# Kernel tuning notes

Hardware: AMD Instinct MI355X
Metric: run time of the kernel (lower is better)

The kernel has to match this reference:

```python
import jax, jax.numpy as jnp
import numpy as np

N = 100000
E = 1600000
IN_C, HID_C, OUT_C = 128, 128, 64


def setup_inputs() -> dict:
    key = jax.random.key(0)
    ks = jax.random.split(key, 8)
    x = jax.random.normal(ks[0], (N, IN_C), dtype=jnp.float32)
    edge_index = jax.random.randint(ks[1], (2, E), 0, N, dtype=jnp.int64)

    def glorot(k, fan_in, fan_out):
        s = jnp.sqrt(6.0 / (fan_in + fan_out))
        return jax.random.uniform(k, (fan_in, fan_out), jnp.float32, -s, s)

    W1 = glorot(ks[2], IN_C, HID_C)
    b1 = jnp.zeros((HID_C,), jnp.float32)
    W2 = glorot(ks[3], HID_C, HID_C)
    b2 = jnp.zeros((HID_C,), jnp.float32)
    W3 = glorot(ks[4], HID_C, OUT_C)
    b3 = jnp.zeros((OUT_C,), jnp.float32)
    return {"x": x, "edge_index": edge_index,
            "W1": W1, "b1": b1, "W2": W2, "b2": b2, "W3": W3, "b3": b3}


def _gcn_norm(row, col, n_nodes):
    # symmetric normalization, add_self_loops=False (PyG gcn_norm)
    deg = jax.ops.segment_sum(jnp.ones(row.shape[0], jnp.float32), col, num_segments=n_nodes)
    dinv = jnp.where(deg > 0, jax.lax.rsqrt(jnp.maximum(deg, 1.0)), 0.0)
    dinv = jnp.where(deg > 0, deg ** -0.5, 0.0)
    return dinv[row] * dinv[col]  # [E]


def _gcn_conv(x, row, col, norm, W, b):
    h = x @ W                                # [N, F_out] dense GEMM first (PyG order)
    msg = h[row] * norm[:, None]             # gather + scale, [E, F_out]
    out = jax.ops.segment_sum(msg, col, num_segments=x.shape[0])  # scatter-add
    return out + b


def reference(x, edge_index, W1, b1, W2, b2, W3, b3):
    row, col = edge_index[0], edge_index[1]
    norm = _gcn_norm(row, col, x.shape[0])
    h = jax.nn.relu(_gcn_conv(x, row, col, norm, W1, b1))   # dropout is identity in eval
    h = jax.nn.relu(_gcn_conv(h, row, col, norm, W2, b2))
    out = _gcn_conv(h, row, col, norm, W3, b3)
    return out
```

## Files before the change

### kernel.cpp

```cpp
#include <hip/hip_runtime.h>
#include <hip/hip_bf16.h>
#include <hip/hip_fp16.h>


#define K_DIM 128
#define SCAN_CHUNK 1024

typedef _Float16 f16x8 __attribute__((ext_vector_type(8)));
typedef float f32x4 __attribute__((ext_vector_type(4)));
typedef const __attribute__((address_space(1))) void gbl_void;
typedef __attribute__((address_space(3))) void lds_void;

static inline long long cdiv_ll(long long a, long long b) { return (a + b - 1) / b; }

__global__ __launch_bounds__(256) void count_kernel(const int* __restrict__ col, int* __restrict__ cnt,
                                                    int* __restrict__ rank, int E) {
    int e = blockIdx.x * 256 + threadIdx.x;
    if (e < E) rank[e] = atomicAdd(&cnt[col[e]], 1);
}

__global__ __launch_bounds__(256) void dinv_kernel(const int* __restrict__ cnt, float* __restrict__ dinv, int N) {
    int n = blockIdx.x * 256 + threadIdx.x;
    if (n < N) {
        int d = cnt[n];
        dinv[n] = (d > 0) ? (1.0f / sqrtf((float)d)) : 0.0f;
    }
}

__global__ __launch_bounds__(256) void scan1_kernel(const int* __restrict__ cnt, int* __restrict__ off,
                                                    int* __restrict__ bsum, int N) {
    __shared__ int lds[256];
    const int t = threadIdx.x;
    const int base = blockIdx.x * SCAN_CHUNK;
    int v[4], s = 0;
#pragma unroll
    for (int j = 0; j < 4; ++j) {
        int i = base + t * 4 + j;
        v[j] = (i < N) ? cnt[i] : 0;
        s += v[j];
    }
    lds[t] = s;
    __syncthreads();
    for (int d = 1; d < 256; d <<= 1) {
        int x = (t >= d) ? lds[t - d] : 0;
        __syncthreads();
        lds[t] += x;
        __syncthreads();
    }
    int excl = lds[t] - s;
    if (t == 255) bsum[blockIdx.x] = lds[255];
    int run = excl;
#pragma unroll
    for (int j = 0; j < 4; ++j) {
        int i = base + t * 4 + j;
        if (i < N) off[i] = run;
        run += v[j];
    }
}

__global__ __launch_bounds__(256) void scan2_kernel(int* __restrict__ bsum, int G, int* __restrict__ off,
                                                    int N, int E) {
    __shared__ int lds[256];
    const int t = threadIdx.x;
    int s = (t < G) ? bsum[t] : 0;
    lds[t] = s;
    __syncthreads();
    for (int d = 1; d < 256; d <<= 1) {
        int x = (t >= d) ? lds[t - d] : 0;
        __syncthreads();
        lds[t] += x;
        __syncthreads();
    }
    if (t < G) bsum[t] = lds[t] - s;
    if (t == 0) off[N] = E;
}

__global__ __launch_bounds__(256) void scan3_kernel(int* __restrict__ off, const int* __restrict__ bsum, int N) {
    int add = bsum[blockIdx.x];
    const int base = blockIdx.x * SCAN_CHUNK;
#pragma unroll
    for (int j = 0; j < 4; ++j) {
        int i = base + threadIdx.x * 4 + j;
        if (i < N) off[i] += add;
    }
}

__global__ __launch_bounds__(256) void fill_kernel(const int* __restrict__ row, const int* __restrict__ col,
                                                   const int* __restrict__ off, const int* __restrict__ rank,
                                                   int* __restrict__ csr_row, int E) {
    int e = blockIdx.x * 256 + threadIdx.x;
    if (e < E) {
        int idx = off[col[e]] + rank[e];
        __builtin_nontemporal_store(row[e], &csr_row[idx]);
    }
}

template <int COUT>
__global__ __launch_bounds__(256) void pack_w_kernel(const float* __restrict__ W, _Float16* __restrict__ Wp) {
    constexpr int NT = COUT / 16;
    int t = blockIdx.x * 256 + threadIdx.x;
    if (t >= 4 * NT * 64) return;
    int lane = t & 63;
    int nt = (t >> 6) % NT;
    int kt = t / (64 * NT);
    int c = lane & 15, q = lane >> 4;
    f16x8 v;
#pragma unroll
    for (int j = 0; j < 8; ++j) {
        int k = kt * 32 + q * 8 + j;
        v[j] = (_Float16)W[k * COUT + nt * 16 + c];
    }
    *(f16x8*)&Wp[(size_t)t * 8] = v;
}

template <int COUT, bool AF16>
__global__ __launch_bounds__(256) void gemm_mfma(const void* __restrict__ Av, const _Float16* __restrict__ Wp,
                                                 const float* __restrict__ dinv, _Float16* __restrict__ Cmat, int M) {
    constexpr int NT = COUT / 16;
    constexpr int NFRAG = 4 * NT * 64;
    __shared__ _Float16 Wlds[NFRAG * 8];

    const int t = threadIdx.x;
    for (int i = t; i < NFRAG; i += 256)
        *(f16x8*)&Wlds[(size_t)i * 8] = *(const f16x8*)&Wp[(size_t)i * 8];
    __syncthreads();

    const int lane = t & 63;
    const int wave = t >> 6;
    const int c = lane & 15;
    const int q = lane >> 4;
    const int row_base = blockIdx.x * 128 + wave * 32;

    f32x4 acc[2][NT];
#pragma unroll
    for (int rt = 0; rt < 2; ++rt)
#pragma unroll
        for (int nt = 0; nt < NT; ++nt) {
            acc[rt][nt][0] = 0.f; acc[rt][nt][1] = 0.f;
            acc[rt][nt][2] = 0.f; acc[rt][nt][3] = 0.f;
        }

#pragma unroll
    for (int kt = 0; kt < 4; ++kt) {
        f16x8 a[2];
#pragma unroll
        for (int rt = 0; rt < 2; ++rt) {
            int r = row_base + rt * 16 + c;
            r = (r < M) ? r : (M - 1);
            if (AF16) {
                const _Float16* Ap = (const _Float16*)Av;
                a[rt] = *(const f16x8*)&Ap[(size_t)r * K_DIM + kt * 32 + q * 8];
            } else {
                const float* ap = (const float*)Av + (size_t)r * K_DIM + kt * 32 + q * 8;
                float4 v0 = *(const float4*)ap;
                float4 v1 = *(const float4*)(ap + 4);
                f16x8 av;
                av[0] = (_Float16)v0.x; av[1] = (_Float16)v0.y;
                av[2] = (_Float16)v0.z; av[3] = (_Float16)v0.w;
                av[4] = (_Float16)v1.x; av[5] = (_Float16)v1.y;
                av[6] = (_Float16)v1.z; av[7] = (_Float16)v1.w;
                a[rt] = av;
            }
        }
#pragma unroll
        for (int nt = 0; nt < NT; ++nt) {
            f16x8 b = *(const f16x8*)&Wlds[(size_t)((kt * NT + nt) * 64 + lane) * 8];
            acc[0][nt] = __builtin_amdgcn_mfma_f32_16x16x32_f16(a[0], b, acc[0][nt], 0, 0, 0);
            acc[1][nt] = __builtin_amdgcn_mfma_f32_16x16x32_f16(a[1], b, acc[1][nt], 0, 0, 0);
        }
    }

#pragma unroll
    for (int rt = 0; rt < 2; ++rt)
#pragma unroll
        for (int reg = 0; reg < 4; ++reg) {
            int row = row_base + rt * 16 + q * 4 + reg;
            if (row < M) {
                float dv = dinv[row];
#pragma unroll
                for (int nt = 0; nt < NT; ++nt)
                    Cmat[(size_t)row * COUT + nt * 16 + c] = (_Float16)(acc[rt][nt][reg] * dv);
            }
        }
}

template <int COUT, bool RELU, typename OutT>
__global__ __launch_bounds__(256) void gather_row(const _Float16* __restrict__ g, const int* __restrict__ off,
                                                  const int* __restrict__ csr_row, const float* __restrict__ dinv,
                                                  const float* __restrict__ bias, OutT* __restrict__ outp, int N) {
    constexpr int TPN = COUT / 8;
    constexpr int NTILE = 256 / TPN;
    constexpr int CH = 16384 / COUT;
    constexpr int EPI = 256 / TPN;
    constexpr int EPW = 64 / TPN;
    __shared__ _Float16 feat[CH * COUT];
    __shared__ int off_s[NTILE + 1];

    const int t = threadIdx.x;
    const int node0 = blockIdx.x * NTILE;

    if (t <= NTILE) {
        int idx = node0 + t;
        off_s[t] = off[idx < N ? idx : N];
    }
    __syncthreads();

    const int j = t % TPN;
    const int n_loc = t / TPN;
    const int w = t >> 6;
    const int node = node0 + n_loc;
    const bool valid = node < N;
    const int sn0 = off_s[n_loc];
    const int sn1 = off_s[n_loc + 1];
    const int s_begin = off_s[0];
    const int s_end = off_s[NTILE];

    float acc[8];
#pragma unroll
    for (int k = 0; k < 8; ++k) acc[k] = 0.f;

    for (int cs = s_begin; cs < s_end; cs += CH) {
        const int ce = (cs + CH < s_end) ? (cs + CH) : s_end;
        const int cnt = ce - cs;
        const int kmax = (cnt + EPI - 1) / EPI;
        for (int k = 0; k < kmax; ++k) {
            int i = k * EPI + n_loc;
            if (i < cnt) {
                int r = csr_row[cs + i];
                const _Float16* src = g + (size_t)r * COUT + j * 8;
                __builtin_amdgcn_global_load_lds((gbl_void*)src,
                                                 (lds_void*)&feat[(size_t)(k * EPI + w * EPW) * COUT],
                                                 16, 0, 0);
            }
        }
        __syncthreads();
        const int lo_s = (sn0 > cs) ? sn0 : cs;
        const int hi_s = (sn1 < ce) ? sn1 : ce;
        for (int s = lo_s; s < hi_s; ++s) {
            f16x8 v = *(const f16x8*)&feat[(size_t)(s - cs) * COUT + j * 8];
#pragma unroll
            for (int k = 0; k < 8; ++k) acc[k] += (float)v[k];
        }
        __syncthreads();
    }

    if (valid) {
        float dv = dinv[node];
        float o[8];
#pragma unroll
        for (int k = 0; k < 8; ++k) {
            o[k] = acc[k] * dv + bias[j * 8 + k];
            if (RELU) o[k] = fmaxf(o[k], 0.f);
        }
        if constexpr (sizeof(OutT) == 2) {
            f16x8 h;
#pragma unroll
            for (int k = 0; k < 8; ++k) h[k] = (_Float16)o[k];
            *(f16x8*)((_Float16*)outp + (size_t)node * COUT + j * 8) = h;
        } else {
            float* op = (float*)outp + (size_t)node * COUT + j * 8;
            *(float4*)op = make_float4(o[0], o[1], o[2], o[3]);
            *(float4*)(op + 4) = make_float4(o[4], o[5], o[6], o[7]);
        }
    }
}

extern "C" void kernel_launch(void* const* d_in, const int* in_sizes, int n_in,
                              void* d_out, int out_size, void* d_ws, size_t ws_size,
                              hipStream_t stream) {
    const float* x  = (const float*)d_in[0];
    const int*   ei = (const int*)d_in[1];
    const float* W1 = (const float*)d_in[2];
    const float* b1 = (const float*)d_in[3];
    const float* W2 = (const float*)d_in[4];
    const float* b2 = (const float*)d_in[5];
    const float* W3 = (const float*)d_in[6];
    const float* b3 = (const float*)d_in[7];

    const int N = in_sizes[0] / 128;
    const int E = in_sizes[1] / 2;
    const int* row = ei;
    const int* col = ei + E;
    const int G = (int)cdiv_ll(N, SCAN_CHUNK);

    char* wsb = (char*)d_ws;
    int*      cnt     = (int*)wsb;      wsb += (size_t)N * 4;
    float*    dinv    = (float*)wsb;    wsb += (size_t)N * 4;
    int*      off     = (int*)wsb;      wsb += (size_t)(N + 1) * 4;
    int*      bsum    = (int*)wsb;      wsb += 256 * 4;
    int*      rank    = (int*)wsb;      wsb += (size_t)E * 4;
    int*      csr_row = (int*)wsb;      wsb += (size_t)E * 4;
    wsb = (char*)((((uintptr_t)wsb) + 15) & ~(uintptr_t)15);
    _Float16* Wp1     = (_Float16*)wsb; wsb += 16384 * 2;
    _Float16* Wp2     = (_Float16*)wsb; wsb += 16384 * 2;
    _Float16* Wp3     = (_Float16*)wsb; wsb += 8192 * 2;
    _Float16* bufA    = (_Float16*)wsb; wsb += (size_t)N * 128 * 2;
    _Float16* bufB    = (_Float16*)wsb;
    float*    out     = (float*)d_out;

    hipMemsetAsync(cnt, 0, (size_t)N * 4, stream);
    count_kernel<<<cdiv_ll(E, 256), 256, 0, stream>>>(col, cnt, rank, E);
    dinv_kernel<<<cdiv_ll(N, 256), 256, 0, stream>>>(cnt, dinv, N);
    scan1_kernel<<<G, 256, 0, stream>>>(cnt, off, bsum, N);
    scan2_kernel<<<1, 256, 0, stream>>>(bsum, G, off, N, E);
    scan3_kernel<<<G, 256, 0, stream>>>(off, bsum, N);
    fill_kernel<<<cdiv_ll(E, 256), 256, 0, stream>>>(row, col, off, rank, csr_row, E);
    pack_w_kernel<128><<<8, 256, 0, stream>>>(W1, Wp1);
    pack_w_kernel<128><<<8, 256, 0, stream>>>(W2, Wp2);
    pack_w_kernel<64><<<4, 256, 0, stream>>>(W3, Wp3);

    const long long gemmBlocks = cdiv_ll(N, 128);

    gemm_mfma<128, false><<<gemmBlocks, 256, 0, stream>>>(x, Wp1, dinv, bufA, N);
    gather_row<128, true, _Float16><<<cdiv_ll(N, 16), 256, 0, stream>>>(bufA, off, csr_row, dinv, b1, bufB, N);

    gemm_mfma<128, true><<<gemmBlocks, 256, 0, stream>>>(bufB, Wp2, dinv, bufA, N);
    gather_row<128, true, _Float16><<<cdiv_ll(N, 16), 256, 0, stream>>>(bufA, off, csr_row, dinv, b2, bufB, N);

    gemm_mfma<64, true><<<gemmBlocks, 256, 0, stream>>>(bufB, Wp3, dinv, bufA, N);
    gather_row<64, false, float><<<cdiv_ll(N, 32), 256, 0, stream>>>(bufA, off, csr_row, dinv, b3, out, N);
}
```

Measured before the change: 517.4 us.

## Split features into 32-wide planes for gather and GEMM intermediate layout

```diff
diff --git a/kernel.cpp b/kernel.cpp
--- a/kernel.cpp
+++ b/kernel.cpp
@@ -149,7 +149,7 @@
             r = (r < M) ? r : (M - 1);
             if (AF16) {
                 const _Float16* Ap = (const _Float16*)Av;
-                a[rt] = *(const f16x8*)&Ap[(size_t)r * K_DIM + kt * 32 + q * 8];
+                a[rt] = *(const f16x8*)&Ap[((size_t)kt * M + r) * 32 + q * 8];
             } else {
                 const float* ap = (const float*)Av + (size_t)r * K_DIM + kt * 32 + q * 8;
                 float4 v0 = *(const float4*)ap;
@@ -179,25 +179,25 @@
                 float dv = dinv[row];
 #pragma unroll
                 for (int nt = 0; nt < NT; ++nt)
-                    Cmat[(size_t)row * COUT + nt * 16 + c] = (_Float16)(acc[rt][nt][reg] * dv);
+                    Cmat[((size_t)(nt >> 1) * M + row) * 32 + (nt & 1) * 16 + c] =
+                        (_Float16)(acc[rt][nt][reg] * dv);
             }
         }
 }
 
-template <int COUT, bool RELU, typename OutT>
-__global__ __launch_bounds__(256) void gather_row(const _Float16* __restrict__ g, const int* __restrict__ off,
-                                                  const int* __restrict__ csr_row, const float* __restrict__ dinv,
-                                                  const float* __restrict__ bias, OutT* __restrict__ outp, int N) {
-    constexpr int TPN = COUT / 8;
-    constexpr int NTILE = 256 / TPN;
-    constexpr int CH = 16384 / COUT;
-    constexpr int EPI = 256 / TPN;
-    constexpr int EPW = 64 / TPN;
-    __shared__ _Float16 feat[CH * COUT];
+template <int NP, bool RELU, typename OutT>
+__global__ __launch_bounds__(256) void gather_sp(const _Float16* __restrict__ g, const int* __restrict__ off,
+                                                 const int* __restrict__ csr_row, const float* __restrict__ dinv,
+                                                 const float* __restrict__ bias, OutT* __restrict__ outp, int N) {
+    constexpr int NTILE = 64;
+    constexpr int CH = 448;
+    __shared__ _Float16 feat[CH * 32];
     __shared__ int off_s[NTILE + 1];
 
     const int t = threadIdx.x;
-    const int node0 = blockIdx.x * NTILE;
+    const int plane = blockIdx.x % NP;
+    const int node0 = (blockIdx.x / NP) * NTILE;
+    const _Float16* gp = g + (size_t)plane * N * 32;
 
     if (t <= NTILE) {
         int idx = node0 + t;
@@ -205,9 +205,10 @@
     }
     __syncthreads();
 
-    const int j = t % TPN;
-    const int n_loc = t / TPN;
+    const int u = t & 3;
+    const int n_loc = t >> 2;
     const int w = t >> 6;
+    const int l = t & 63;
     const int node = node0 + n_loc;
     const bool valid = node < N;
     const int sn0 = off_s[n_loc];
@@ -222,14 +223,15 @@
     for (int cs = s_begin; cs < s_end; cs += CH) {
         const int ce = (cs + CH < s_end) ? (cs + CH) : s_end;
         const int cnt = ce - cs;
-        const int kmax = (cnt + EPI - 1) / EPI;
+        const int kmax = (cnt + 63) >> 6;
         for (int k = 0; k < kmax; ++k) {
-            int i = k * EPI + n_loc;
+            int i = k * 64 + w * 16 + (l >> 2);
             if (i < cnt) {
                 int r = csr_row[cs + i];
-                const _Float16* src = g + (size_t)r * COUT + j * 8;
+                int us = (l & 3) ^ (i & 3);
+                const _Float16* src = gp + (size_t)r * 32 + us * 8;
                 __builtin_amdgcn_global_load_lds((gbl_void*)src,
-                                                 (lds_void*)&feat[(size_t)(k * EPI + w * EPW) * COUT],
+                                                 (lds_void*)&feat[((size_t)k * 64 + w * 16) * 32],
                                                  16, 0, 0);
             }
         }
@@ -237,7 +239,8 @@
         const int lo_s = (sn0 > cs) ? sn0 : cs;
         const int hi_s = (sn1 < ce) ? sn1 : ce;
         for (int s = lo_s; s < hi_s; ++s) {
-            f16x8 v = *(const f16x8*)&feat[(size_t)(s - cs) * COUT + j * 8];
+            int i = s - cs;
+            f16x8 v = *(const f16x8*)&feat[(size_t)i * 32 + ((u ^ (i & 3)) * 8)];
 #pragma unroll
             for (int k = 0; k < 8; ++k) acc[k] += (float)v[k];
         }
@@ -249,16 +252,16 @@
         float o[8];
 #pragma unroll
         for (int k = 0; k < 8; ++k) {
-            o[k] = acc[k] * dv + bias[j * 8 + k];
+            o[k] = acc[k] * dv + bias[plane * 32 + u * 8 + k];
             if (RELU) o[k] = fmaxf(o[k], 0.f);
         }
         if constexpr (sizeof(OutT) == 2) {
             f16x8 h;
 #pragma unroll
             for (int k = 0; k < 8; ++k) h[k] = (_Float16)o[k];
-            *(f16x8*)((_Float16*)outp + (size_t)node * COUT + j * 8) = h;
+            *(f16x8*)((_Float16*)outp + ((size_t)plane * N + node) * 32 + u * 8) = h;
         } else {
-            float* op = (float*)outp + (size_t)node * COUT + j * 8;
+            float* op = (float*)outp + (size_t)node * 64 + plane * 32 + u * 8;
             *(float4*)op = make_float4(o[0], o[1], o[2], o[3]);
             *(float4*)(op + 4) = make_float4(o[4], o[5], o[6], o[7]);
         }
@@ -310,13 +313,14 @@
     pack_w_kernel<64><<<4, 256, 0, stream>>>(W3, Wp3);
 
     const long long gemmBlocks = cdiv_ll(N, 128);
+    const long long nb         = cdiv_ll(N, 64);
 
     gemm_mfma<128, false><<<gemmBlocks, 256, 0, stream>>>(x, Wp1, dinv, bufA, N);
-    gather_row<128, true, _Float16><<<cdiv_ll(N, 16), 256, 0, stream>>>(bufA, off, csr_row, dinv, b1, bufB, N);
+    gather_sp<4, true, _Float16><<<nb * 4, 256, 0, stream>>>(bufA, off, csr_row, dinv, b1, bufB, N);
 
     gemm_mfma<128, true><<<gemmBlocks, 256, 0, stream>>>(bufB, Wp2, dinv, bufA, N);
-    gather_row<128, true, _Float16><<<cdiv_ll(N, 16), 256, 0, stream>>>(bufA, off, csr_row, dinv, b2, bufB, N);
+    gather_sp<4, true, _Float16><<<nb * 4, 256, 0, stream>>>(bufA, off, csr_row, dinv, b2, bufB, N);
 
     gemm_mfma<64, true><<<gemmBlocks, 256, 0, stream>>>(bufB, Wp3, dinv, bufA, N);
-    gather_row<64, false, float><<<cdiv_ll(N, 32), 256, 0, stream>>>(bufA, off, csr_row, dinv, b3, out, N);
-}
+    gather_sp<2, false, float><<<nb * 2, 256, 0, stream>>>(bufA, off, csr_row, dinv, b3, out, N);
+}
```

Result: no change. 521.6 us (+0.8%).
